# Performance work log

Measured on AMD Instinct MI355X. Metric: run time of the kernel, lower is better.

The kernel has to match this reference:

```python
import jax, jax.numpy as jnp
import numpy as np

B, T = 64, 32768
N_PROT = 18          # protein channels (len(steady_state))
N_PROLIF = 12        # prolif-hill library terms
N_LIN = 18           # lin-hill library terms (== len(sigmoid_sign))
N_TERMS = 1 + N_PROLIF + N_LIN  # 31


def setup_inputs() -> dict:
    key = jax.random.key(0)
    ks = jax.random.split(key, 8)
    candidates = jax.random.uniform(ks[0], (B, T, 4 + N_PROT), dtype=jnp.float32)
    a = jax.random.normal(ks[1], (N_TERMS,), dtype=jnp.float32)
    steady_state = jax.random.uniform(ks[2], (N_PROT,), dtype=jnp.float32) * 0.5
    # +/-1 signs, mimicking the hard-coded sign vector in the original module
    sigmoid_sign = jnp.where(
        jax.random.bernoulli(ks[3], 0.5, (N_LIN,)), 1.0, -1.0
    ).astype(jnp.float32)
    K1 = jnp.array([0.5], dtype=jnp.float32)
    theta = jnp.array([2.0], dtype=jnp.float32)
    K2 = jnp.array([0.3], dtype=jnp.float32)
    # library indices: cols 0,1 of prolif and col 0 of lin index x (4 channels);
    # col 2 of prolif and col 1 of lin index proteins (18 channels)
    prolif_hill_idx = jnp.stack(
        [
            jax.random.randint(ks[4], (N_PROLIF,), 0, 4),
            jax.random.randint(jax.random.fold_in(ks[4], 1), (N_PROLIF,), 0, 4),
            jax.random.randint(jax.random.fold_in(ks[4], 2), (N_PROLIF,), 0, N_PROT),
        ],
        axis=1,
    ).astype(jnp.int32)
    lin_hill_idx = jnp.stack(
        [
            jax.random.randint(ks[5], (N_LIN,), 0, 4),
            jax.random.randint(jax.random.fold_in(ks[5], 1), (N_LIN,), 0, N_PROT),
        ],
        axis=1,
    ).astype(jnp.int32)
    self_propagate = jax.random.bernoulli(ks[6], 0.5, (N_TERMS,))
    return {
        "candidates": candidates,
        "a": a,
        "steady_state": steady_state,
        "sigmoid_sign": sigmoid_sign,
        "K1": K1,
        "theta": theta,
        "K2": K2,
        "prolif_hill_idx": prolif_hill_idx,
        "lin_hill_idx": lin_hill_idx,
        "self_propagate": self_propagate,
    }


def reference(candidates, a, steady_state, sigmoid_sign, K1, theta, K2,
              prolif_hill_idx, lin_hill_idx, self_propagate):
    con = candidates[:, :, 0:1]                       # [B,T,1]
    x3 = candidates[:, :, 1:4]                        # [B,T,3]
    proteins = candidates[:, :, 4:]                   # [B,T,18]
    d_prot = proteins - steady_state                  # [B,T,18]
    # augment x with its sum -> 4 channels
    x = jnp.concatenate([x3, jnp.sum(x3, axis=2, keepdims=True)], axis=2)

    # prolif-hill terms: Log_term(x_i, x_j) * Hill(K1, protein_k)
    p0 = x[:, :, prolif_hill_idx[:, 0]]
    p1 = x[:, :, prolif_hill_idx[:, 1]]
    p2 = proteins[:, :, prolif_hill_idx[:, 2]]
    prolif_hill = p0 * (1.0 - p1 / theta) * (p2 / (K1 + p2))  # [B,T,12]

    # lin-hill terms: x_i * Hill(K2, |d_prot_j|) * sharp_sigmoid(sign * d_prot_j)
    l0 = x[:, :, lin_hill_idx[:, 0]]
    dp = d_prot[:, :, lin_hill_idx[:, 1]]
    adp = jnp.abs(dp)
    sig = jax.nn.sigmoid(500.0 * (sigmoid_sign * dp - 0.05))
    lin_hill = l0 * (adp / (K2 + adp)) * sig                  # [B,T,18]

    terms = jnp.concatenate([con, prolif_hill, lin_hill], axis=2)  # [B,T,31]

    # masked zero-out: keep term i iff (self_propagate[i] and a[i] >= 0)
    # or (not self_propagate[i] and a[i] <= 0)
    keep = jnp.where(self_propagate, a >= 0.0, a <= 0.0)
    terms = terms * keep.astype(terms.dtype)

    return terms @ a  # [B,T]
```

## Files before the change

kernel.cpp:

```cpp
#include <hip/hip_runtime.h>

#define B_ 64
#define T_ 32768
#define NPROT 18
#define NPROLIF 12
#define NLIN 18
#define ROW 22
#define BLK 256
#define F4_PER_BLK (BLK*ROW/4)

__global__ __launch_bounds__(BLK) void sindy_kernel(
    const float* __restrict__ cand,
    const float* __restrict__ a,
    const float* __restrict__ ss,
    const float* __restrict__ sgn,
    const float* __restrict__ K1p,
    const float* __restrict__ thetap,
    const float* __restrict__ K2p,
    const int* __restrict__ pidx,
    const int* __restrict__ lidx,
    const int* __restrict__ sprop,
    float* __restrict__ out)
{
    __shared__ float sRow[BLK*ROW];
    __shared__ float sX[BLK*5];
    __shared__ uint2 sPP[NPROLIF];
    __shared__ uint4 sLP[NLIN];
    __shared__ float sScal[4];

    const int tid = threadIdx.x;

    if (tid < NPROLIF) {
        int i = tid;
        int ia = pidx[i*3+0], ib = pidx[i*3+1], ic = pidx[i*3+2];
        float av = a[1+i];
        bool keep = sprop[1+i] ? (av >= 0.f) : (av <= 0.f);
        unsigned offs = (unsigned)(ia*4) | ((unsigned)(ib*4) << 8) | ((unsigned)(16 + ic*4) << 16);
        sPP[i] = make_uint2(offs, __float_as_uint(keep ? av : 0.f));
    } else if (tid < NPROLIF + NLIN) {
        int j = tid - NPROLIF;
        int i0 = lidx[j*2+0], i1 = lidx[j*2+1];
        float av = a[1+NPROLIF+j];
        bool keep = sprop[1+NPROLIF+j] ? (av >= 0.f) : (av <= 0.f);
        unsigned offs = (unsigned)(i0*4) | ((unsigned)(16 + i1*4) << 8);
        sLP[j] = make_uint4(offs,
                            __float_as_uint(keep ? av : 0.f),
                            __float_as_uint(500.f * sgn[j]),
                            __float_as_uint(ss[i1]));
    } else if (tid == NPROLIF + NLIN) {
        float av = a[0];
        bool keep = sprop[0] ? (av >= 0.f) : (av <= 0.f);
        sScal[0] = K1p[0];
        sScal[1] = 1.0f / thetap[0];
        sScal[2] = K2p[0];
        sScal[3] = keep ? av : 0.f;
    }

    const float4* g4 = reinterpret_cast<const float4*>(cand)
                       + (long long)blockIdx.x * F4_PER_BLK;
    float4* s4 = reinterpret_cast<float4*>(sRow);
    #pragma unroll
    for (int k = 0; k < 5; ++k) s4[tid + k*BLK] = g4[tid + k*BLK];
    if (tid < F4_PER_BLK - 5*BLK) s4[tid + 5*BLK] = g4[tid + 5*BLK];

    __syncthreads();

    const char* row = (const char*)&sRow[tid*ROW];
    float x0 = sRow[tid*ROW+1], x1 = sRow[tid*ROW+2], x2 = sRow[tid*ROW+3];
    float xs = x0 + x1 + x2;
    float* xr = &sX[tid*5];
    xr[0] = x0; xr[1] = x1; xr[2] = x2; xr[3] = xs;
    const char* xrow = (const char*)xr;

    const float K1 = sScal[0], invTh = sScal[1], K2 = sScal[2];
    float acc = sScal[3] * sRow[tid*ROW+0];

    #pragma unroll
    for (int i = 0; i < NPROLIF; ++i) {
        uint2 pp = sPP[i];
        float coef = __uint_as_float(pp.y);
        float pA = *(const float*)(xrow + (pp.x & 0xffu));
        float pB = *(const float*)(xrow + ((pp.x >> 8) & 0xffu));
        float pC = *(const float*)(row + (pp.x >> 16));
        float h  = pC * __builtin_amdgcn_rcpf(K1 + pC);
        acc += coef * (pA * (1.0f - pB * invTh) * h);
    }

    #pragma unroll
    for (int j = 0; j < NLIN; ++j) {
        uint4 lp = sLP[j];
        float coef = __uint_as_float(lp.y);
        float A    = __uint_as_float(lp.z);
        float ssv  = __uint_as_float(lp.w);
        float l0 = *(const float*)(xrow + (lp.x & 0xffu));
        float pr = *(const float*)(row + ((lp.x >> 8) & 0xffu));
        float dp  = pr - ssv;
        float adp = fabsf(dp);
        float h   = adp * __builtin_amdgcn_rcpf(K2 + adp);
        float z   = A * dp - 25.0f;
        float e   = __expf(-z);
        float sig = __builtin_amdgcn_rcpf(1.0f + e);
        acc += coef * (l0 * h * sig);
    }

    out[(long long)blockIdx.x * BLK + tid] = acc;
}

extern "C" void kernel_launch(void* const* d_in, const int* in_sizes, int n_in,
                              void* d_out, int out_size, void* d_ws, size_t ws_size,
                              hipStream_t stream) {
    const float* cand = (const float*)d_in[0];
    const float* a    = (const float*)d_in[1];
    const float* ss   = (const float*)d_in[2];
    const float* sgn  = (const float*)d_in[3];
    const float* K1   = (const float*)d_in[4];
    const float* th   = (const float*)d_in[5];
    const float* K2   = (const float*)d_in[6];
    const int*   pidx = (const int*)d_in[7];
    const int*   lidx = (const int*)d_in[8];
    const int*   sp   = (const int*)d_in[9];
    float* out = (float*)d_out;

    const int nblocks = (B_ * T_) / BLK;
    hipLaunchKernelGGL(sindy_kernel, dim3(nblocks), dim3(BLK), 0, stream,
                       cand, a, ss, sgn, K1, th, K2, pidx, lidx, sp, out);
}
```

Before: 43.77 us.

## Use direct global-to-LDS loads and register selects for x channels

Global-to-shared staging of candidate rows now uses the global_load_lds builtin, so data goes straight into LDS without passing through registers. The loads are also issued before the parameter setup, which lets that setup overlap the transfer. The separate sX shared array is removed; the four x values (including their sum) stay in registers and are picked with a two-level select instead of indexed LDS reads. This cuts LDS traffic and VGPR use for the staging, at the cost of a few extra select instructions per term.

```diff
diff --git a/kernel.cpp b/kernel.cpp
--- a/kernel.cpp
+++ b/kernel.cpp
@@ -8,6 +8,15 @@
 #define ROW 22
 #define BLK 256
 #define F4_PER_BLK (BLK*ROW/4)
+
+#define AS1 __attribute__((address_space(1)))
+#define AS3 __attribute__((address_space(3)))
+
+__device__ __forceinline__ float sel4(unsigned i, float x0, float x1, float x2, float x3) {
+    float lo = (i & 1u) ? x1 : x0;
+    float hi = (i & 1u) ? x3 : x2;
+    return (i & 2u) ? hi : lo;
+}
 
 __global__ __launch_bounds__(BLK) void sindy_kernel(
     const float* __restrict__ cand,
@@ -23,26 +32,41 @@
     float* __restrict__ out)
 {
     __shared__ float sRow[BLK*ROW];
-    __shared__ float sX[BLK*5];
     __shared__ uint2 sPP[NPROLIF];
     __shared__ uint4 sLP[NLIN];
     __shared__ float sScal[4];
 
     const int tid = threadIdx.x;
+    const int wbase = tid & ~63;
+
+    const float4* g4 = reinterpret_cast<const float4*>(cand)
+                       + (long long)blockIdx.x * F4_PER_BLK;
+    float4* s4 = reinterpret_cast<float4*>(sRow);
+    #pragma unroll
+    for (int k = 0; k < 5; ++k) {
+        __builtin_amdgcn_global_load_lds(
+            (const AS1 void*)(g4 + k*BLK + tid),
+            (AS3 void*)(s4 + k*BLK + wbase), 16, 0, 0);
+    }
+    if (tid < F4_PER_BLK - 5*BLK) {
+        __builtin_amdgcn_global_load_lds(
+            (const AS1 void*)(g4 + 5*BLK + tid),
+            (AS3 void*)(s4 + 5*BLK + wbase), 16, 0, 0);
+    }
 
     if (tid < NPROLIF) {
         int i = tid;
         int ia = pidx[i*3+0], ib = pidx[i*3+1], ic = pidx[i*3+2];
         float av = a[1+i];
         bool keep = sprop[1+i] ? (av >= 0.f) : (av <= 0.f);
-        unsigned offs = (unsigned)(ia*4) | ((unsigned)(ib*4) << 8) | ((unsigned)(16 + ic*4) << 16);
+        unsigned offs = (unsigned)ia | ((unsigned)ib << 2) | ((unsigned)(16 + ic*4) << 8);
         sPP[i] = make_uint2(offs, __float_as_uint(keep ? av : 0.f));
     } else if (tid < NPROLIF + NLIN) {
         int j = tid - NPROLIF;
         int i0 = lidx[j*2+0], i1 = lidx[j*2+1];
         float av = a[1+NPROLIF+j];
         bool keep = sprop[1+NPROLIF+j] ? (av >= 0.f) : (av <= 0.f);
-        unsigned offs = (unsigned)(i0*4) | ((unsigned)(16 + i1*4) << 8);
+        unsigned offs = (unsigned)i0 | ((unsigned)(16 + i1*4) << 8);
         sLP[j] = make_uint4(offs,
                             __float_as_uint(keep ? av : 0.f),
                             __float_as_uint(500.f * sgn[j]),
@@ -56,32 +80,25 @@
         sScal[3] = keep ? av : 0.f;
     }
 
-    const float4* g4 = reinterpret_cast<const float4*>(cand)
-                       + (long long)blockIdx.x * F4_PER_BLK;
-    float4* s4 = reinterpret_cast<float4*>(sRow);
-    #pragma unroll
-    for (int k = 0; k < 5; ++k) s4[tid + k*BLK] = g4[tid + k*BLK];
-    if (tid < F4_PER_BLK - 5*BLK) s4[tid + 5*BLK] = g4[tid + 5*BLK];
-
     __syncthreads();
 
     const char* row = (const char*)&sRow[tid*ROW];
-    float x0 = sRow[tid*ROW+1], x1 = sRow[tid*ROW+2], x2 = sRow[tid*ROW+3];
-    float xs = x0 + x1 + x2;
-    float* xr = &sX[tid*5];
-    xr[0] = x0; xr[1] = x1; xr[2] = x2; xr[3] = xs;
-    const char* xrow = (const char*)xr;
+    float con = sRow[tid*ROW+0];
+    float x0  = sRow[tid*ROW+1];
+    float x1  = sRow[tid*ROW+2];
+    float x2  = sRow[tid*ROW+3];
+    float xs  = x0 + x1 + x2;
 
     const float K1 = sScal[0], invTh = sScal[1], K2 = sScal[2];
-    float acc = sScal[3] * sRow[tid*ROW+0];
+    float acc = sScal[3] * con;
 
     #pragma unroll
     for (int i = 0; i < NPROLIF; ++i) {
         uint2 pp = sPP[i];
         float coef = __uint_as_float(pp.y);
-        float pA = *(const float*)(xrow + (pp.x & 0xffu));
-        float pB = *(const float*)(xrow + ((pp.x >> 8) & 0xffu));
-        float pC = *(const float*)(row + (pp.x >> 16));
+        float pA = sel4(pp.x & 3u, x0, x1, x2, xs);
+        float pB = sel4((pp.x >> 2) & 3u, x0, x1, x2, xs);
+        float pC = *(const float*)(row + ((pp.x >> 8) & 0xffu));
         float h  = pC * __builtin_amdgcn_rcpf(K1 + pC);
         acc += coef * (pA * (1.0f - pB * invTh) * h);
     }
@@ -92,7 +109,7 @@
         float coef = __uint_as_float(lp.y);
         float A    = __uint_as_float(lp.z);
         float ssv  = __uint_as_float(lp.w);
-        float l0 = *(const float*)(xrow + (lp.x & 0xffu));
+        float l0 = sel4(lp.x & 3u, x0, x1, x2, xs);
         float pr = *(const float*)(row + ((lp.x >> 8) & 0xffu));
         float dp  = pr - ssv;
         float adp = fabsf(dp);
```

New measurement: 44.62 us. No clear change (+1.9%).

## Load rows straight into LDS per wave and drop shared parameter tables

Applied to the files above, without the earlier changes.

Each wave now copies its own 64 rows from global memory directly into LDS with global_load_lds, using 16-byte and 4-byte transfers. It then waits only on its own outstanding loads, which replaces the block-wide barrier. The per-term parameters (indices, masked coefficients, steady state, sign) now come from uniform global loads inside unrolled loops rather than from LDS tables built by a few threads. The x channel lookup uses register selects instead of indexed LDS reads. The sigmoid slope is built from the sign bit alone, which assumes sigmoid_sign is exactly ±1. Staging data this way cuts VGPR traffic and synchronization in a bandwidth-bound kernel, but it depends on the direct-to-LDS builtins and adds more scalar loads.

```diff
diff --git a/kernel.cpp b/kernel.cpp
--- a/kernel.cpp
+++ b/kernel.cpp
@@ -1,13 +1,19 @@
 #include <hip/hip_runtime.h>
 
-#define B_ 64
-#define T_ 32768
-#define NPROT 18
 #define NPROLIF 12
 #define NLIN 18
 #define ROW 22
 #define BLK 256
-#define F4_PER_BLK (BLK*ROW/4)
+#define NSLAB 8192
+
+#define AS1 __attribute__((address_space(1)))
+#define AS3 __attribute__((address_space(3)))
+
+__device__ __forceinline__ float sel4(unsigned i, float x0, float x1, float x2, float x3) {
+    float lo = (i & 1u) ? x1 : x0;
+    float hi = (i & 1u) ? x3 : x2;
+    return (i & 2u) ? hi : lo;
+}
 
 __global__ __launch_bounds__(BLK) void sindy_kernel(
     const float* __restrict__ cand,
@@ -23,87 +29,70 @@
     float* __restrict__ out)
 {
     __shared__ float sRow[BLK*ROW];
-    __shared__ float sX[BLK*5];
-    __shared__ uint2 sPP[NPROLIF];
-    __shared__ uint4 sLP[NLIN];
-    __shared__ float sScal[4];
 
-    const int tid = threadIdx.x;
+    const int tid  = threadIdx.x;
+    const int wave = tid >> 6;
+    const int lane = tid & 63;
 
-    if (tid < NPROLIF) {
-        int i = tid;
-        int ia = pidx[i*3+0], ib = pidx[i*3+1], ic = pidx[i*3+2];
-        float av = a[1+i];
-        bool keep = sprop[1+i] ? (av >= 0.f) : (av <= 0.f);
-        unsigned offs = (unsigned)(ia*4) | ((unsigned)(ib*4) << 8) | ((unsigned)(16 + ic*4) << 16);
-        sPP[i] = make_uint2(offs, __float_as_uint(keep ? av : 0.f));
-    } else if (tid < NPROLIF + NLIN) {
-        int j = tid - NPROLIF;
-        int i0 = lidx[j*2+0], i1 = lidx[j*2+1];
-        float av = a[1+NPROLIF+j];
-        bool keep = sprop[1+NPROLIF+j] ? (av >= 0.f) : (av <= 0.f);
-        unsigned offs = (unsigned)(i0*4) | ((unsigned)(16 + i1*4) << 8);
-        sLP[j] = make_uint4(offs,
-                            __float_as_uint(keep ? av : 0.f),
-                            __float_as_uint(500.f * sgn[j]),
-                            __float_as_uint(ss[i1]));
-    } else if (tid == NPROLIF + NLIN) {
-        float av = a[0];
-        bool keep = sprop[0] ? (av >= 0.f) : (av <= 0.f);
-        sScal[0] = K1p[0];
-        sScal[1] = 1.0f / thetap[0];
-        sScal[2] = K2p[0];
-        sScal[3] = keep ? av : 0.f;
-    }
+    const float* gw = cand + (size_t)blockIdx.x * (BLK*ROW) + wave * (64*ROW);
+    float* lw = &sRow[wave * (64*ROW)];
+    #pragma unroll
+    for (int k = 0; k < 5; ++k)
+        __builtin_amdgcn_global_load_lds((const AS1 void*)(gw + k*256 + lane*4),
+                                         (AS3 void*)(lw + k*256), 16, 0, 0);
+    #pragma unroll
+    for (int j = 0; j < 2; ++j)
+        __builtin_amdgcn_global_load_lds((const AS1 void*)(gw + 1280 + j*64 + lane),
+                                         (AS3 void*)(lw + 1280 + j*64), 4, 0, 0);
 
-    const float4* g4 = reinterpret_cast<const float4*>(cand)
-                       + (long long)blockIdx.x * F4_PER_BLK;
-    float4* s4 = reinterpret_cast<float4*>(sRow);
-    #pragma unroll
-    for (int k = 0; k < 5; ++k) s4[tid + k*BLK] = g4[tid + k*BLK];
-    if (tid < F4_PER_BLK - 5*BLK) s4[tid + 5*BLK] = g4[tid + 5*BLK];
+    asm volatile("s_waitcnt vmcnt(0)" ::: "memory");
+    __builtin_amdgcn_sched_barrier(0);
 
-    __syncthreads();
+    const float* row = &sRow[tid*ROW];
+    float con = row[0], x0 = row[1], x1 = row[2], x2 = row[3];
+    float xs  = x0 + x1 + x2;
 
-    const char* row = (const char*)&sRow[tid*ROW];
-    float x0 = sRow[tid*ROW+1], x1 = sRow[tid*ROW+2], x2 = sRow[tid*ROW+3];
-    float xs = x0 + x1 + x2;
-    float* xr = &sX[tid*5];
-    xr[0] = x0; xr[1] = x1; xr[2] = x2; xr[3] = xs;
-    const char* xrow = (const char*)xr;
+    const float K1    = K1p[0];
+    const float invTh = __builtin_amdgcn_rcpf(thetap[0]);
+    const float K2    = K2p[0];
 
-    const float K1 = sScal[0], invTh = sScal[1], K2 = sScal[2];
-    float acc = sScal[3] * sRow[tid*ROW+0];
+    auto coefFor = [&](int k) -> float {
+        unsigned avb  = __float_as_uint(a[k]);
+        unsigned keep = ((sprop[k] != 0) ? 1u : 0u) ^ (avb >> 31);
+        return __uint_as_float(keep ? avb : 0u);
+    };
+
+    float acc = coefFor(0) * con;
 
     #pragma unroll
-    for (int i = 0; i < NPROLIF; ++i) {
-        uint2 pp = sPP[i];
-        float coef = __uint_as_float(pp.y);
-        float pA = *(const float*)(xrow + (pp.x & 0xffu));
-        float pB = *(const float*)(xrow + ((pp.x >> 8) & 0xffu));
-        float pC = *(const float*)(row + (pp.x >> 16));
+    for (int t = 0; t < NPROLIF; ++t) {
+        float coef = coefFor(1 + t);
+        int ia = pidx[t*3+0], ib = pidx[t*3+1], ic = pidx[t*3+2];
+        float pA = sel4((unsigned)ia, x0, x1, x2, xs);
+        float pB = sel4((unsigned)ib, x0, x1, x2, xs);
+        float pC = row[4 + ic];
         float h  = pC * __builtin_amdgcn_rcpf(K1 + pC);
         acc += coef * (pA * (1.0f - pB * invTh) * h);
     }
 
     #pragma unroll
-    for (int j = 0; j < NLIN; ++j) {
-        uint4 lp = sLP[j];
-        float coef = __uint_as_float(lp.y);
-        float A    = __uint_as_float(lp.z);
-        float ssv  = __uint_as_float(lp.w);
-        float l0 = *(const float*)(xrow + (lp.x & 0xffu));
-        float pr = *(const float*)(row + ((lp.x >> 8) & 0xffu));
+    for (int t = 0; t < NLIN; ++t) {
+        float coef = coefFor(1 + NPROLIF + t);
+        int i0 = lidx[t*2+0], i1 = lidx[t*2+1];
+        float A   = __uint_as_float(0x43fa0000u  |
+                                    (__float_as_uint(sgn[t]) & 0x80000000u));
+        float ssv = ss[i1];
+        float l0  = sel4((unsigned)i0, x0, x1, x2, xs);
+        float pr  = row[4 + i1];
         float dp  = pr - ssv;
         float adp = fabsf(dp);
         float h   = adp * __builtin_amdgcn_rcpf(K2 + adp);
-        float z   = A * dp - 25.0f;
-        float e   = __expf(-z);
+        float e   = __expf(-(A * dp - 25.0f));
         float sig = __builtin_amdgcn_rcpf(1.0f + e);
         acc += coef * (l0 * h * sig);
     }
 
-    out[(long long)blockIdx.x * BLK + tid] = acc;
+    out[(size_t)blockIdx.x * BLK + tid] = acc;
 }
 
 extern "C" void kernel_launch(void* const* d_in, const int* in_sizes, int n_in,
@@ -121,7 +110,6 @@
     const int*   sp   = (const int*)d_in[9];
     float* out = (float*)d_out;
 
-    const int nblocks = (B_ * T_) / BLK;
-    hipLaunchKernelGGL(sindy_kernel, dim3(nblocks), dim3(BLK), 0, stream,
+    hipLaunchKernelGGL(sindy_kernel, dim3(NSLAB), dim3(BLK), 0, stream,
                        cand, a, ss, sgn, K1, th, K2, pidx, lidx, sp, out);
 }
```

Result: slower. 60.16 us (+37.4%).
